# Kernel tuning notes

Measured on AMD Instinct MI355X. Metric: run time of the kernel, lower is better.

## Reference

```python
import jax, jax.numpy as jnp
import numpy as np

B, T, N, F = 16, 64, 5000, 1
E = 80000
HG, HT = 64, 128


def setup_inputs() -> dict:
    key = jax.random.key(0)
    ks = jax.random.split(key, 20)
    p = lambda i, shape: jax.random.normal(ks[i], shape, jnp.float32) * 0.05
    return {
        "x_seq": jax.random.normal(ks[0], (B, T, N, F), jnp.float32),
        "edge_index": jax.random.randint(ks[1], (2, E), 0, N, jnp.int64 if jax.config.jax_enable_x64 else jnp.int32),
        # SAGEConv 1: out = mean_agg(x_j) @ Wl + b + x_i @ Wr  (PyG lin_l has bias, lin_r none)
        "s1_Wl": p(2, (F, HG)), "s1_Wr": p(3, (F, HG)), "s1_b": jnp.zeros((HG,), jnp.float32),
        "s2_Wl": p(4, (HG, HG)), "s2_Wr": p(5, (HG, HG)), "s2_b": jnp.zeros((HG,), jnp.float32),
        # GRU (torch layout): W_ih [3H, in], W_hh [3H, H], gates ordered r,z,n
        "gru_Wih": p(6, (3 * HT, HG)), "gru_Whh": p(7, (3 * HT, HT)),
        "gru_bih": jnp.zeros((3 * HT,), jnp.float32), "gru_bhh": jnp.zeros((3 * HT,), jnp.float32),
        # head: Linear(HT,64) -> ReLU -> Linear(64,1)
        "h1_W": p(8, (HT, 64)), "h1_b": jnp.zeros((64,), jnp.float32),
        "h2_W": p(9, (64, 1)), "h2_b": jnp.zeros((1,), jnp.float32),
    }


def reference(x_seq, edge_index, s1_Wl, s1_Wr, s1_b, s2_Wl, s2_Wr, s2_b,
              gru_Wih, gru_Whh, gru_bih, gru_bhh, h1_W, h1_b, h2_W, h2_b):
    src, dst = edge_index[0], edge_index[1]
    # in-degree for mean aggregation (clamped to 1 like PyG mean aggr)
    deg = jax.ops.segment_sum(jnp.ones(src.shape, jnp.float32), dst, num_segments=N)
    inv_deg = (1.0 / jnp.maximum(deg, 1.0))[:, None]  # [N,1]

    def sage(x, Wl, Wr, b):  # x: [B, N, d]
        msg = x[:, src]  # gather source features: [B, E, d]
        agg = jax.vmap(lambda m: jax.ops.segment_sum(m, dst, num_segments=N))(msg)
        agg = agg * inv_deg  # mean over incoming edges
        return agg @ Wl + x @ Wr + b

    def conv_step(_, x_t):  # x_t: [B, N, F]
        h = jax.nn.relu(sage(x_t, s1_Wl, s1_Wr, s1_b))
        h = jax.nn.relu(sage(h, s2_Wl, s2_Wr, s2_b))
        return None, h.mean(axis=1)  # global mean pool -> [B, HG]

    _, outs = jax.lax.scan(conv_step, None, jnp.moveaxis(x_seq, 1, 0))  # [T, B, HG]

    def gru_step(h, x_t):  # h: [B, HT], x_t: [B, HG]
        gi = x_t @ gru_Wih.T + gru_bih
        gh = h @ gru_Whh.T + gru_bhh
        ir, iz, i_n = jnp.split(gi, 3, axis=-1)
        hr, hz, hn = jnp.split(gh, 3, axis=-1)
        r = jax.nn.sigmoid(ir + hr)
        z = jax.nn.sigmoid(iz + hz)
        n = jnp.tanh(i_n + r * hn)
        h_new = (1.0 - z) * n + z * h
        return h_new, None

    h0 = jnp.zeros((x_seq.shape[0], HT), x_seq.dtype)
    hT, _ = jax.lax.scan(gru_step, h0, outs)  # last hidden state == H[:, -1, :]

    out = jax.nn.relu(hT @ h1_W + h1_b) @ h2_W + h2_b  # [B, 1]
    return out[:, 0]
```

## Files before the change

### kernel.cpp

```cpp
#include <hip/hip_runtime.h>

#define NN 5000
#define EE 80000
#define BB 16
#define TT 64

constexpr int ECAP2 = 2048;

typedef float  f32x2 __attribute__((ext_vector_type(2)));
typedef float  f32x4 __attribute__((ext_vector_type(4)));
typedef short  short8 __attribute__((ext_vector_type(8)));

__device__ inline unsigned short f2bf(float f) {
  unsigned int u = __builtin_bit_cast(unsigned int, f);
  u = (u + 0x7fffu + ((u >> 16) & 1u)) >> 16;
  return (unsigned short)u;
}
__device__ inline float bf2f(unsigned short h) {
  unsigned int u = ((unsigned int)h) << 16;
  return __builtin_bit_cast(float, u);
}
__device__ inline int swz(int i) { return i ^ ((i >> 4) & 31); }

__global__ void k_deg(const int* __restrict__ dst, int* __restrict__ deg) {
  int e = blockIdx.x * 256 + threadIdx.x;
  if (e < EE) atomicAdd(&deg[dst[e]], 1);
}

__global__ __launch_bounds__(1024) void k_sort(const int* __restrict__ deg,
                                               int* __restrict__ perm,
                                               int* __restrict__ rank) {
  __shared__ int hist[256];
  int t = threadIdx.x;
  if (t < 256) hist[t] = 0;
  __syncthreads();
  for (int n = t; n < NN; n += 1024) atomicAdd(&hist[min(deg[n], 255)], 1);
  __syncthreads();
  if (t == 0) { int run = 0; for (int d = 0; d < 256; ++d) { int c = hist[d]; hist[d] = run; run += c; } }
  __syncthreads();
  for (int n = t; n < NN; n += 1024) {
    int d = min(deg[n], 255);
    int p = atomicAdd(&hist[d], 1);
    perm[p] = n;
    rank[n] = p;
  }
}

__global__ __launch_bounds__(1024) void k_scan(const int* __restrict__ deg,
                                               const int* __restrict__ perm,
                                               int* __restrict__ rowptrP,
                                               float* __restrict__ invdegP) {
  __shared__ int part[1024];
  int t = threadIdx.x;
  const int CH = 5;
  int base = t * CH;
  int cnt[CH];
  int s = 0;
  for (int i = 0; i < CH; ++i) {
    int idx = base + i;
    int d = (idx < NN) ? deg[perm[idx]] : 0;
    cnt[i] = d; s += d;
  }
  part[t] = s;
  __syncthreads();
  for (int off = 1; off < 1024; off <<= 1) {
    int v = (t >= off) ? part[t - off] : 0;
    __syncthreads();
    part[t] += v;
    __syncthreads();
  }
  int run = part[t] - s;
  for (int i = 0; i < CH; ++i) {
    int idx = base + i;
    if (idx < NN) {
      rowptrP[idx] = run;
      invdegP[idx] = 1.0f / fmaxf((float)cnt[i], 1.0f);
      run += cnt[i];
    }
  }
  if (t == 0) rowptrP[NN] = EE;
}

__global__ void k_fill(const int* __restrict__ src, const int* __restrict__ dst,
                       const int* __restrict__ rowptrP, const int* __restrict__ rank,
                       int* __restrict__ fill, int* __restrict__ col) {
  int e = blockIdx.x * 256 + threadIdx.x;
  if (e < EE) {
    int r = rank[dst[e]];
    int p = atomicAdd(&fill[r], 1);
    col[rowptrP[r] + p] = src[e];
  }
}

__global__ __launch_bounds__(256) void k_axp(const float* __restrict__ xseq,
                                             const int* __restrict__ rowptrP,
                                             const int* __restrict__ colg,
                                             const float* __restrict__ invdegP,
                                             const int* __restrict__ perm,
                                             float2* __restrict__ axp) {
  int q = blockIdx.x;
  __shared__ float xl[NN];
  const float* xs = xseq + (size_t)q * NN;
  for (int i = threadIdx.x; i < NN; i += 256) xl[i] = xs[i];
  __syncthreads();
  for (int ii = threadIdx.x; ii < NN; ii += 256) {
    int r0 = rowptrP[ii], r1 = rowptrP[ii + 1];
    float s = 0.f;
    for (int i = r0; i < r1; ++i) s += xl[colg[i]];
    int pn = perm[ii];
    axp[(size_t)q * NN + pn] = make_float2(s * invdegP[ii], xl[pn]);
  }
}

__global__ void k_wsplit(const float* __restrict__ Wl2, const float* __restrict__ Wr2,
                         unsigned short* __restrict__ Bfh, unsigned short* __restrict__ Bfl) {
  int t = blockIdx.x * 256 + threadIdx.x;
  if (t >= 16 * 64) return;
  int frag = t >> 6, lane = t & 63;
  int ks = frag >> 2, tn = frag & 3;
  int nlo = lane & 15, lg = lane >> 4;
  #pragma unroll
  for (int i = 0; i < 8; ++i) {
    int k = ks * 32 + lg * 8 + i;
    int n = tn * 16 + nlo;
    float v = (k < 64) ? Wl2[k * 64 + n] : Wr2[(k - 64) * 64 + n];
    unsigned short h = f2bf(v);
    unsigned short l = f2bf(v - bf2f(h));
    Bfh[(size_t)t * 8 + i] = h;
    Bfl[(size_t)t * 8 + i] = l;
  }
}

__global__ __launch_bounds__(256, 4) void k_conv2(const float2* __restrict__ axp,
    const int* __restrict__ rowptrP, const int* __restrict__ colg,
    const float* __restrict__ invdegP, const int* __restrict__ perm,
    const float* __restrict__ wl1, const float* __restrict__ wr1, const float* __restrict__ b1,
    const unsigned short* __restrict__ Bfh, const unsigned short* __restrict__ Bfl,
    const float* __restrict__ b2,
    float* __restrict__ outs)
{
  __shared__ __align__(16) unsigned int At[64 * 65];
  __shared__ __align__(16) float2 eb[ECAP2];
  __shared__ float ps[4 * 64];
  const int q  = blockIdx.y;
  const int n0 = blockIdx.x * 64;
  const int tid = threadIdx.x;
  const int w = tid >> 6, lane = tid & 63;
  const float2* ax = axp + (size_t)q * NN;

  const int slot = n0 + lane;
  const int r0 = rowptrP[min(slot, NN)];
  const int r1 = rowptrP[min(slot + 1, NN)];
  const int e0 = __builtin_amdgcn_readfirstlane(r0);
  const int e1 = __builtin_amdgcn_readfirstlane(rowptrP[min(n0 + 64, NN)]);
  const int eblk = e1 - e0;

  for (int i = tid; i < eblk; i += 256)
    if (i < ECAP2) eb[swz(i)] = ax[colg[e0 + i]];
  __syncthreads();

  f32x2 wl2[8], wr2[8], bb2[8];
  {
    const float4* wl4 = (const float4*)(wl1 + 16 * w);
    const float4* wr4 = (const float4*)(wr1 + 16 * w);
    const float4* b4  = (const float4*)(b1  + 16 * w);
    #pragma unroll
    for (int j = 0; j < 4; ++j) {
      float4 a = wl4[j], b = wr4[j], c = b4[j];
      wl2[2*j] = {a.x, a.y}; wl2[2*j+1] = {a.z, a.w};
      wr2[2*j] = {b.x, b.y}; wr2[2*j+1] = {b.z, b.w};
      bb2[2*j] = {c.x, c.y}; bb2[2*j+1] = {c.z, c.w};
    }
  }
  f32x2 acc2[8];
  #pragma unroll
  for (int j = 0; j < 8; ++j) acc2[j] = {0.f, 0.f};

  const int dg = r1 - r0;
  const int i0 = r0 - e0;
  if (eblk <= ECAP2) {
    int bi = min(i0, ECAP2 - 1);
    float2 p = eb[swz(bi)];
    for (int e = 0; e < dg; ++e) {
      float2 cur = p;
      int nx = min(i0 + e + 1, ECAP2 - 1);
      p = eb[swz(nx)];
      f32x2 ca = {cur.x, cur.x}, cx = {cur.y, cur.y};
      #pragma unroll
      for (int j = 0; j < 8; ++j) {
        f32x2 z = __builtin_elementwise_fma(ca, wl2[j],
                  __builtin_elementwise_fma(cx, wr2[j], bb2[j]));
        acc2[j] += __builtin_elementwise_max(z, (f32x2)(0.f));
      }
    }
  } else {
    for (int e = 0; e < dg; ++e) {
      int bi = i0 + e;
      float2 cur = (bi < ECAP2) ? eb[swz(bi)] : ax[colg[r0 + e]];
      f32x2 ca = {cur.x, cur.x}, cx = {cur.y, cur.y};
      #pragma unroll
      for (int j = 0; j < 8; ++j) {
        f32x2 z = __builtin_elementwise_fma(ca, wl2[j],
                  __builtin_elementwise_fma(cx, wr2[j], bb2[j]));
        acc2[j] += __builtin_elementwise_max(z, (f32x2)(0.f));
      }
    }
  }

  {
    const float iv = invdegP[min(slot, NN - 1)];
    const f32x2 iv2 = {iv, iv};
    #pragma unroll
    for (int j = 0; j < 8; ++j) {
      f32x2 a = acc2[j] * iv2;
      #pragma unroll
      for (int h = 0; h < 2; ++h) {
        float v = a[h];
        unsigned short hi = f2bf(v);
        unsigned short lo = f2bf(v - bf2f(hi));
        At[(16 * w + 2 * j + h) * 65 + lane] = ((unsigned int)hi << 16) | lo;
      }
    }
  }
  __syncthreads();

  const int nlo = lane & 15, lg = lane >> 4;
  const int gslot = n0 + w * 16 + nlo;
  const bool valid = gslot < NN;
  float2 own = make_float2(0.f, 0.f);
  if (valid) own = ax[perm[gslot]];
  f32x4 acc[4] = {{0.f,0.f,0.f,0.f},{0.f,0.f,0.f,0.f},{0.f,0.f,0.f,0.f},{0.f,0.f,0.f,0.f}};

  #pragma unroll 1
  for (int ks = 0; ks < 2; ++ks) {
    unsigned int u[8];
    #pragma unroll
    for (int i = 0; i < 8; ++i)
      u[i] = At[(ks * 32 + lg * 8 + i) * 65 + w * 16 + nlo];
    int4 ah, al;
    ah.x = __builtin_amdgcn_perm(u[1], u[0], 0x07060302u);
    ah.y = __builtin_amdgcn_perm(u[3], u[2], 0x07060302u);
    ah.z = __builtin_amdgcn_perm(u[5], u[4], 0x07060302u);
    ah.w = __builtin_amdgcn_perm(u[7], u[6], 0x07060302u);
    al.x = __builtin_amdgcn_perm(u[1], u[0], 0x05040100u);
    al.y = __builtin_amdgcn_perm(u[3], u[2], 0x05040100u);
    al.z = __builtin_amdgcn_perm(u[5], u[4], 0x05040100u);
    al.w = __builtin_amdgcn_perm(u[7], u[6], 0x05040100u);
    short8 ah8 = __builtin_bit_cast(short8, ah);
    short8 al8 = __builtin_bit_cast(short8, al);
    const short8* bh = (const short8*)(Bfh + (size_t)ks * 4 * 64 * 8);
    const short8* bl = (const short8*)(Bfl + (size_t)ks * 4 * 64 * 8);
    #pragma unroll
    for (int tn = 0; tn < 4; ++tn) {
      short8 bhv = bh[tn * 64 + lane];
      short8 blv = bl[tn * 64 + lane];
      acc[tn] = __builtin_amdgcn_mfma_f32_16x16x32_bf16(al8, bhv, acc[tn], 0, 0, 0);
      acc[tn] = __builtin_amdgcn_mfma_f32_16x16x32_bf16(ah8, blv, acc[tn], 0, 0, 0);
      acc[tn] = __builtin_amdgcn_mfma_f32_16x16x32_bf16(ah8, bhv, acc[tn], 0, 0, 0);
    }
  }

  #pragma unroll 1
  for (int ks = 2; ks < 4; ++ks) {
    const int kb = (ks - 2) * 32 + lg * 8;
    float4 wa0 = *(const float4*)(wl1 + kb), wa1 = *(const float4*)(wl1 + kb + 4);
    float4 wb0 = *(const float4*)(wr1 + kb), wb1 = *(const float4*)(wr1 + kb + 4);
    float4 bc0 = *(const float4*)(b1 + kb),  bc1 = *(const float4*)(b1 + kb + 4);
    float hv[8];
    hv[0] = fmaxf(fmaf(own.x, wa0.x, fmaf(own.y, wb0.x, bc0.x)), 0.f);
    hv[1] = fmaxf(fmaf(own.x, wa0.y, fmaf(own.y, wb0.y, bc0.y)), 0.f);
    hv[2] = fmaxf(fmaf(own.x, wa0.z, fmaf(own.y, wb0.z, bc0.z)), 0.f);
    hv[3] = fmaxf(fmaf(own.x, wa0.w, fmaf(own.y, wb0.w, bc0.w)), 0.f);
    hv[4] = fmaxf(fmaf(own.x, wa1.x, fmaf(own.y, wb1.x, bc1.x)), 0.f);
    hv[5] = fmaxf(fmaf(own.x, wa1.y, fmaf(own.y, wb1.y, bc1.y)), 0.f);
    hv[6] = fmaxf(fmaf(own.x, wa1.z, fmaf(own.y, wb1.z, bc1.z)), 0.f);
    hv[7] = fmaxf(fmaf(own.x, wa1.w, fmaf(own.y, wb1.w, bc1.w)), 0.f);
    int4 ah, al;
    unsigned int hh[8], ll[8];
    #pragma unroll
    for (int i = 0; i < 8; ++i) {
      unsigned short h = f2bf(hv[i]);
      hh[i] = h;
      ll[i] = f2bf(hv[i] - bf2f(h));
    }
    ah.x = (int)((hh[1] << 16) | hh[0]); ah.y = (int)((hh[3] << 16) | hh[2]);
    ah.z = (int)((hh[5] << 16) | hh[4]); ah.w = (int)((hh[7] << 16) | hh[6]);
    al.x = (int)((ll[1] << 16) | ll[0]); al.y = (int)((ll[3] << 16) | ll[2]);
    al.z = (int)((ll[5] << 16) | ll[4]); al.w = (int)((ll[7] << 16) | ll[6]);
    short8 ah8 = __builtin_bit_cast(short8, ah);
    short8 al8 = __builtin_bit_cast(short8, al);
    const short8* bh = (const short8*)(Bfh + (size_t)ks * 4 * 64 * 8);
    const short8* bl = (const short8*)(Bfl + (size_t)ks * 4 * 64 * 8);
    #pragma unroll
    for (int tn = 0; tn < 4; ++tn) {
      short8 bhv = bh[tn * 64 + lane];
      short8 blv = bl[tn * 64 + lane];
      acc[tn] = __builtin_amdgcn_mfma_f32_16x16x32_bf16(al8, bhv, acc[tn], 0, 0, 0);
      acc[tn] = __builtin_amdgcn_mfma_f32_16x16x32_bf16(ah8, blv, acc[tn], 0, 0, 0);
      acc[tn] = __builtin_amdgcn_mfma_f32_16x16x32_bf16(ah8, bhv, acc[tn], 0, 0, 0);
    }
  }

  #pragma unroll
  for (int tn = 0; tn < 4; ++tn) {
    const float bias = b2[tn * 16 + nlo];
    float s = 0.f;
    #pragma unroll
    for (int r = 0; r < 4; ++r) {
      int nslot = n0 + w * 16 + lg * 4 + r;
      float v = fmaxf(acc[tn][r] + bias, 0.f);
      if (nslot < NN) s += v;
    }
    s += __shfl_xor(s, 16, 64);
    s += __shfl_xor(s, 32, 64);
    if (lg == 0) ps[w * 64 + tn * 16 + nlo] = s;
  }
  __syncthreads();
  if (tid < 64) {
    float t = ps[tid] + ps[64 + tid] + ps[128 + tid] + ps[192 + tid];
    int b = q / TT, tt = q % TT;
    atomicAdd(&outs[((size_t)tt * BB + b) * 64 + tid], t);
  }
}

__global__ void k_T(const float* __restrict__ Wih, const float* __restrict__ Whh,
                    float* __restrict__ WihT, float* __restrict__ WhhT) {
  int id = blockIdx.x * 256 + threadIdx.x;
  if (id < 384 * 64)  { int r = id / 64;  int c = id % 64;  WihT[c * 384 + r] = Wih[id]; }
  if (id < 384 * 128) { int r = id / 128; int c = id % 128; WhhT[c * 384 + r] = Whh[id]; }
}

__global__ __launch_bounds__(384) void k_gi(const float* __restrict__ outs,
                                            const float* __restrict__ WihT,
                                            const float* __restrict__ bih,
                                            float* __restrict__ gi) {
  int g = blockIdx.x;
  __shared__ float xl[64];
  int r = threadIdx.x;
  if (r < 64) xl[r] = outs[(size_t)g * 64 + r] * (1.0f / (float)NN);
  __syncthreads();
  float acc = bih[r];
  #pragma unroll 8
  for (int c = 0; c < 64; ++c) acc = fmaf(WihT[c * 384 + r], xl[c], acc);
  gi[(size_t)g * 384 + r] = acc;
}

__global__ __launch_bounds__(384) void k_gru(const float* __restrict__ gi,
                                             const float* __restrict__ WhhT,
                                             const float* __restrict__ bhh,
                                             const float* __restrict__ h1W,
                                             const float* __restrict__ h1b,
                                             const float* __restrict__ h2W,
                                             const float* __restrict__ h2b,
                                             float* __restrict__ out) {
  int b = blockIdx.x, r = threadIdx.x;
  __shared__ float hl[128];
  __shared__ float ghl[384];
  __shared__ float t1l[64];
  float wreg[128];
  #pragma unroll
  for (int c = 0; c < 128; ++c) wreg[c] = WhhT[c * 384 + r];
  float bh = bhh[r];
  if (r < 128) hl[r] = 0.f;
  __syncthreads();
  for (int t = 0; t < TT; ++t) {
    float acc = bh;
    #pragma unroll
    for (int c = 0; c < 128; ++c) acc = fmaf(wreg[c], hl[c], acc);
    ghl[r] = acc;
    __syncthreads();
    if (r < 128) {
      const float* gio = gi + ((size_t)t * BB + b) * 384;
      float ir = gio[r], iz = gio[128 + r], inn = gio[256 + r];
      float hr = ghl[r], hz = ghl[128 + r], hn = ghl[256 + r];
      float rg = 1.f / (1.f + expf(-(ir + hr)));
      float zg = 1.f / (1.f + expf(-(iz + hz)));
      float ng = tanhf(inn + rg * hn);
      hl[r] = (1.f - zg) * ng + zg * hl[r];
    }
    __syncthreads();
  }
  if (r < 64) {
    float a = h1b[r];
    #pragma unroll
    for (int c = 0; c < 128; ++c) a = fmaf(hl[c], h1W[c * 64 + r], a);
    t1l[r] = fmaxf(a, 0.f);
  }
  __syncthreads();
  if (r == 0) {
    float o = h2b[0];
    for (int j = 0; j < 64; ++j) o = fmaf(t1l[j], h2W[j], o);
    out[b] = o;
  }
}

extern "C" void kernel_launch(void* const* d_in, const int* in_sizes, int n_in,
                              void* d_out, int out_size, void* d_ws, size_t ws_size,
                              hipStream_t stream) {
  const float* xseq = (const float*)d_in[0];
  const int*   ei   = (const int*)d_in[1];
  const float* s1Wl = (const float*)d_in[2];
  const float* s1Wr = (const float*)d_in[3];
  const float* s1b  = (const float*)d_in[4];
  const float* s2Wl = (const float*)d_in[5];
  const float* s2Wr = (const float*)d_in[6];
  const float* s2b  = (const float*)d_in[7];
  const float* gWih = (const float*)d_in[8];
  const float* gWhh = (const float*)d_in[9];
  const float* gbih = (const float*)d_in[10];
  const float* gbhh = (const float*)d_in[11];
  const float* h1W  = (const float*)d_in[12];
  const float* h1b  = (const float*)d_in[13];
  const float* h2W  = (const float*)d_in[14];
  const float* h2b  = (const float*)d_in[15];
  float* out = (float*)d_out;

  char* ws = (char*)d_ws;
  int*    deg     = (int*)(ws + 0);
  int*    fill    = (int*)(ws + 20480);
  float*  outs    = (float*)(ws + 40960);
  int*    rowptrP = (int*)(ws + 303104);
  float*  invdegP = (float*)(ws + 323584);
  int*    col     = (int*)(ws + 344064);
  int*    perm    = (int*)(ws + 664576);
  int*    rank    = (int*)(ws + 685056);
  float2* axp     = (float2*)(ws + 705536);
  float*  WihT    = (float*)(ws + 41665536);
  float*  WhhT    = (float*)(ws + 41763840);
  float*  gi      = (float*)(ws + 41960448);
  unsigned short* Bfh = (unsigned short*)(ws + 43533312);
  unsigned short* Bfl = (unsigned short*)(ws + 43549696);

  const int* srcI = ei;
  const int* dstI = ei + EE;

  hipMemsetAsync(d_ws, 0, 303104, stream);
  k_deg  <<<(EE + 255) / 256, 256, 0, stream>>>(dstI, deg);
  k_sort <<<1, 1024, 0, stream>>>(deg, perm, rank);
  k_scan <<<1, 1024, 0, stream>>>(deg, perm, rowptrP, invdegP);
  k_fill <<<(EE + 255) / 256, 256, 0, stream>>>(srcI, dstI, rowptrP, rank, fill, col);
  k_wsplit<<<4, 256, 0, stream>>>(s2Wl, s2Wr, Bfh, Bfl);
  k_axp  <<<BB * TT, 256, 0, stream>>>(xseq, rowptrP, col, invdegP, perm, axp);
  dim3 g2(79, BB * TT);
  k_conv2<<<g2, 256, 0, stream>>>(axp, rowptrP, col, invdegP, perm,
                                  s1Wl, s1Wr, s1b, Bfh, Bfl, s2b, outs);
  k_T    <<<192, 256, 0, stream>>>(gWih, gWhh, WihT, WhhT);
  k_gi   <<<BB * TT, 384, 0, stream>>>(outs, WihT, gbih, gi);
  k_gru  <<<BB, 384, 0, stream>>>(gi, WhhT, gbhh, h1W, h1b, h2W, h2b, out);
}
```

Measured before the change: 1.151 ms.

## Shrink conv2 LDS footprint and read edge pairs as float4 from shared buffer

```diff
diff --git a/kernel.cpp b/kernel.cpp
--- a/kernel.cpp
+++ b/kernel.cpp
@@ -5,7 +5,7 @@
 #define BB 16
 #define TT 64
 
-constexpr int ECAP2 = 2048;
+constexpr int ECAP2 = 1952;
 
 typedef float  f32x2 __attribute__((ext_vector_type(2)));
 typedef float  f32x4 __attribute__((ext_vector_type(4)));
@@ -20,7 +20,7 @@
   unsigned int u = ((unsigned int)h) << 16;
   return __builtin_bit_cast(float, u);
 }
-__device__ inline int swz(int i) { return i ^ ((i >> 4) & 31); }
+__device__ inline int swz2(int i) { return i ^ (((i >> 5) & 15) << 1); }
 
 __global__ void k_deg(const int* __restrict__ dst, int* __restrict__ deg) {
   int e = blockIdx.x * 256 + threadIdx.x;
@@ -141,7 +141,7 @@
 {
   __shared__ __align__(16) unsigned int At[64 * 65];
   __shared__ __align__(16) float2 eb[ECAP2];
-  __shared__ float ps[4 * 64];
+  float* ps = (float*)At;
   const int q  = blockIdx.y;
   const int n0 = blockIdx.x * 64;
   const int tid = threadIdx.x;
@@ -154,9 +154,12 @@
   const int e0 = __builtin_amdgcn_readfirstlane(r0);
   const int e1 = __builtin_amdgcn_readfirstlane(rowptrP[min(n0 + 64, NN)]);
   const int eblk = e1 - e0;
-
-  for (int i = tid; i < eblk; i += 256)
-    if (i < ECAP2) eb[swz(i)] = ax[colg[e0 + i]];
+  const bool fits = eblk <= ECAP2;
+
+  if (fits) {
+    for (int i = tid; i < eblk; i += 256)
+      eb[swz2(i)] = ax[colg[e0 + i]];
+  }
   __syncthreads();
 
   f32x2 wl2[8], wr2[8], bb2[8];
@@ -176,34 +179,46 @@
   #pragma unroll
   for (int j = 0; j < 8; ++j) acc2[j] = {0.f, 0.f};
 
+  auto edge1 = [&](float a, float x) {
+    f32x2 ca = {a, a}, cx = {x, x};
+    #pragma unroll
+    for (int j = 0; j < 8; ++j) {
+      f32x2 z = __builtin_elementwise_fma(ca, wl2[j],
+                __builtin_elementwise_fma(cx, wr2[j], bb2[j]));
+      acc2[j] += __builtin_elementwise_max(z, (f32x2)(0.f));
+    }
+  };
+
   const int dg = r1 - r0;
-  const int i0 = r0 - e0;
-  if (eblk <= ECAP2) {
-    int bi = min(i0, ECAP2 - 1);
-    float2 p = eb[swz(bi)];
-    for (int e = 0; e < dg; ++e) {
-      float2 cur = p;
-      int nx = min(i0 + e + 1, ECAP2 - 1);
-      p = eb[swz(nx)];
-      f32x2 ca = {cur.x, cur.x}, cx = {cur.y, cur.y};
+  if (fits) {
+    int i = r0 - e0;
+    int rem = dg;
+    if ((i & 1) && rem) {
+      float2 ab = eb[swz2(i)];
+      edge1(ab.x, ab.y);
+      ++i; --rem;
+    }
+    for (; rem >= 2; rem -= 2, i += 2) {
+      float4 v = *(const float4*)&eb[swz2(i)];
+      f32x2 a0 = {v.x, v.x}, x0 = {v.y, v.y}, a1 = {v.z, v.z}, x1 = {v.w, v.w};
       #pragma unroll
       for (int j = 0; j < 8; ++j) {
-        f32x2 z = __builtin_elementwise_fma(ca, wl2[j],
-                  __builtin_elementwise_fma(cx, wr2[j], bb2[j]));
-        acc2[j] += __builtin_elementwise_max(z, (f32x2)(0.f));
+        f32x2 z0 = __builtin_elementwise_fma(a0, wl2[j],
+                   __builtin_elementwise_fma(x0, wr2[j], bb2[j]));
+        f32x2 z1 = __builtin_elementwise_fma(a1, wl2[j],
+                   __builtin_elementwise_fma(x1, wr2[j], bb2[j]));
+        acc2[j] += __builtin_elementwise_max(z0, (f32x2)(0.f))
+                 + __builtin_elementwise_max(z1, (f32x2)(0.f));
       }
+    }
+    if (rem) {
+      float2 ab = eb[swz2(i)];
+      edge1(ab.x, ab.y);
     }
   } else {
     for (int e = 0; e < dg; ++e) {
-      int bi = i0 + e;
-      float2 cur = (bi < ECAP2) ? eb[swz(bi)] : ax[colg[r0 + e]];
-      f32x2 ca = {cur.x, cur.x}, cx = {cur.y, cur.y};
-      #pragma unroll
-      for (int j = 0; j < 8; ++j) {
-        f32x2 z = __builtin_elementwise_fma(ca, wl2[j],
-                  __builtin_elementwise_fma(cx, wr2[j], bb2[j]));
-        acc2[j] += __builtin_elementwise_max(z, (f32x2)(0.f));
-      }
+      float2 ab = ax[colg[r0 + e]];
+      edge1(ab.x, ab.y);
     }
   }
 
@@ -300,6 +315,7 @@
       acc[tn] = __builtin_amdgcn_mfma_f32_16x16x32_bf16(ah8, bhv, acc[tn], 0, 0, 0);
     }
   }
+  __syncthreads();
 
   #pragma unroll
   for (int tn = 0; tn < 4; ++tn) {
```

Measured after the change: 1.140 ms. About the same (-1.0%).
